# Optimization experiments

Measured on AMD Instinct MI355X. Metric: run time of the kernel, lower is better.

The kernel has to match this reference:

```python
import jax, jax.numpy as jnp
import numpy as np

BATCH, T, IN_DIM = 256, 1024, 96
N_UNITS, N_CLASSES = 256, 10
EPS, BETA, GAMMA = 0.01, 0.5, 0.0


def setup_inputs() -> dict:
    key = jax.random.key(0)
    k = jax.random.split(key, 7)
    # Xavier-ish scales for linear layers; unit gaussian for C, B (gaussian_init_ std=1)
    return {
        "x":   jax.random.normal(k[0], (BATCH, T, IN_DIM), dtype=jnp.float32),
        "E_w": jax.random.normal(k[1], (N_UNITS, IN_DIM), dtype=jnp.float32) * (2.0 / (IN_DIM + N_UNITS)) ** 0.5,
        "E_b": jnp.zeros((N_UNITS,), dtype=jnp.float32),
        "C":   jax.random.normal(k[2], (N_UNITS, N_UNITS), dtype=jnp.float32) / N_UNITS ** 0.5,
        "B":   jax.random.normal(k[3], (N_UNITS, N_UNITS), dtype=jnp.float32) / N_UNITS ** 0.5,
        "D_w": jax.random.normal(k[4], (N_CLASSES, N_UNITS), dtype=jnp.float32) * (2.0 / (N_UNITS + N_CLASSES)) ** 0.5,
        "D_b": jnp.zeros((N_CLASSES,), dtype=jnp.float32),
    }


def reference(x, E_w, E_b, C, B, D_w, D_b):
    # Invariant recurrence matrices (the torch code rebuilds these every step)
    I = jnp.eye(N_UNITS, dtype=x.dtype)
    A  = BETA * (C - C.T) + (1.0 - BETA) * (C + C.T) - GAMMA * I
    Dm = BETA * (B - B.T) + (1.0 - BETA) * (B + B.T) - GAMMA * I

    # Input projection for all timesteps at once: [B, T, N]
    z = jnp.einsum("btf,nf->btn", x, E_w) + E_b

    def step(h, z_t):  # h: [B, N], z_t: [B, N]
        h = h + EPS * (h @ Dm) + EPS * jnp.tanh(h @ A + z_t)
        return h, None

    h0 = jnp.zeros((x.shape[0], N_UNITS), dtype=x.dtype)
    h, _ = jax.lax.scan(step, h0, jnp.swapaxes(z, 0, 1))  # scan over T

    return h @ D_w.T + D_b  # [B, n_classes]
```

## Files before the change

### kernel.cpp

```cpp
#include <hip/hip_runtime.h>

#define BATCH 256
#define TT 1024
#define IN_DIM 96
#define NU 256
#define NC 10
#define EPS 0.01f
#define BETA 0.5f
#define GAMMA 0.0f

typedef _Float16 f16x8 __attribute__((ext_vector_type(8)));
typedef float f32x4 __attribute__((ext_vector_type(4)));

#define ZP_BYTES ((size_t)TT * BATCH * NU * 2)
#define WSW_OFF  ZP_BYTES
#define WSW_BYTES ((size_t)16384 * 16)
#define ESW_OFF  (WSW_OFF + WSW_BYTES)

__global__ void prep_w(const float* __restrict__ C, const float* __restrict__ B,
                       _Float16* __restrict__ Wsw) {
    int u = blockIdx.x * 256 + threadIdx.x;
    int l = u & 63;
    int i = (u >> 6) & 1;
    int c = (u >> 7) & 7;
    int mat = (u >> 10) & 1;
    int w = u >> 11;
    int n = w * 32 + i * 16 + (l & 15);
    int kb = c * 32 + (l >> 4) * 8;
    const float* M = mat ? C : B;
    float scale = mat ? 16.0f : EPS;
    f16x8 v;
#pragma unroll
    for (int j = 0; j < 8; j++) {
        int k = kb + j;
        float m1 = M[k * NU + n];
        float m2 = M[n * NU + k];
        float val = BETA * (m1 - m2) + (1.0f - BETA) * (m1 + m2)
                    - ((k == n) ? GAMMA : 0.0f);
        v[j] = (_Float16)(val * scale);
    }
    ((f16x8*)Wsw)[u] = v;
}

__global__ void prep_e(const float* __restrict__ Ew, _Float16* __restrict__ Esw) {
    int u = blockIdx.x * 256 + threadIdx.x;
    int l = u & 63;
    int i = (u >> 6) & 3;
    int wc = u >> 8;
    int c = wc % 3;
    int w = wc / 3;
    int n = w * 64 + i * 16 + (l & 15);
    int kb = c * 32 + (l >> 4) * 8;
    f16x8 v;
#pragma unroll
    for (int j = 0; j < 8; j++)
        v[j] = (_Float16)Ew[n * IN_DIM + kb + j];
    ((f16x8*)Esw)[u] = v;
}

__global__ __launch_bounds__(256) void zproj(const float* __restrict__ x,
                                             const float* __restrict__ Eb,
                                             const _Float16* __restrict__ Esw,
                                             _Float16* __restrict__ zp) {
    __shared__ __align__(16) _Float16 xh[64 * 104];
    __shared__ float eb[NU];
    int tid = threadIdx.x;
    int l = tid & 63, w = tid >> 6, m = l & 15, quad = l >> 4;
    size_t R0 = (size_t)blockIdx.x * 64;

    const float* xb = x + R0 * IN_DIM;
#pragma unroll
    for (int it = 0; it < 24; it++) {
        int idx = tid + it * 256;
        int r = idx / 96, k = idx - r * 96;
        xh[r * 104 + k] = (_Float16)xb[idx];
    }
    eb[tid] = Eb[tid];

    f16x8 ef[3][4];
    const f16x8* Ep = (const f16x8*)Esw;
#pragma unroll
    for (int c = 0; c < 3; c++)
#pragma unroll
        for (int i = 0; i < 4; i++)
            ef[c][i] = Ep[((w * 3 + c) * 4 + i) * 64 + l];
    __syncthreads();

    f32x4 zero4 = {0.f, 0.f, 0.f, 0.f};
    f32x4 acc[4][4];
#pragma unroll
    for (int mt = 0; mt < 4; mt++)
#pragma unroll
        for (int i = 0; i < 4; i++) acc[mt][i] = zero4;

#pragma unroll
    for (int mt = 0; mt < 4; mt++) {
#pragma unroll
        for (int c = 0; c < 3; c++) {
            f16x8 af = *(const f16x8*)&xh[(mt * 16 + m) * 104 + c * 32 + quad * 8];
#pragma unroll
            for (int i = 0; i < 4; i++)
                acc[mt][i] = __builtin_amdgcn_mfma_f32_16x16x32_f16(af, ef[c][i],
                                                                    acc[mt][i], 0, 0, 0);
        }
    }

#pragma unroll
    for (int mt = 0; mt < 4; mt++)
#pragma unroll
        for (int i = 0; i < 4; i++) {
            int col = w * 64 + i * 16 + m;
            float ebv = eb[col];
#pragma unroll
            for (int r = 0; r < 4; r++) {
                size_t gr = R0 + (size_t)(mt * 16 + quad * 4 + r);
                size_t b = gr >> 10, t = gr & 1023;
                zp[(t * BATCH + b) * NU + col] = (_Float16)(acc[mt][i][r] + ebv);
            }
        }
}


__device__ __forceinline__ void load_zchunk(_Float16 zb[2][8],
                                            const _Float16* __restrict__ zp,
                                            int tb, int zrow, int colb) {
#pragma unroll
    for (int s = 0; s < 2; s++) {
        int ts = tb + s; ts = (ts > TT - 1) ? TT - 1 : ts;
#pragma unroll
        for (int r = 0; r < 4; r++)
#pragma unroll
            for (int i = 0; i < 2; i++)
                zb[s][i * 4 + r] = zp[((size_t)ts * 256 + zrow + r) * 256 + colb + i * 16];
    }
}

__device__ __forceinline__ void step_fn(const _Float16* __restrict__ hb,
                                        _Float16* __restrict__ hn,
                                        const f16x8 wd[8][2], const f16x8 wa[8][2],
                                        float hm[8], const _Float16 zs[8],
                                        int m, int q, int w) {
    f32x4 faccD[2], faccA[2];
    f32x4 zero4 = {0.f, 0.f, 0.f, 0.f};
#pragma unroll
    for (int i = 0; i < 2; i++) {
        faccD[i] = zero4;
        f32x4 zi = {(float)zs[i * 4 + 0], (float)zs[i * 4 + 1],
                    (float)zs[i * 4 + 2], (float)zs[i * 4 + 3]};
        faccA[i] = zi;
    }

#pragma unroll
    for (int c = 0; c < 8; c++) {
        f16x8 af = *(const f16x8*)&hb[m * 264 + c * 32 + q * 8];
#pragma unroll
        for (int i = 0; i < 2; i++) {
            faccD[i] = __builtin_amdgcn_mfma_f32_16x16x32_f16(af, wd[c][i], faccD[i], 0, 0, 0);
            faccA[i] = __builtin_amdgcn_mfma_f32_16x16x32_f16(af, wa[c][i], faccA[i], 0, 0, 0);
        }
    }

#pragma unroll
    for (int i = 0; i < 2; i++) {
        int n = w * 32 + i * 16 + m;
#pragma unroll
        for (int r = 0; r < 4; r++) {
            int row = q * 4 + r;
            float xin = faccA[i][r];
            float e = __builtin_amdgcn_exp2f(xin * 2.8853900817779268f);
            float th = 1.0f - 2.0f * __builtin_amdgcn_rcpf(e + 1.0f);
            hm[i * 4 + r] += faccD[i][r] + (EPS * 0.0625f) * th;
            hn[row * 264 + n] = (_Float16)hm[i * 4 + r];
        }
    }
    __syncthreads();
}

__global__ __launch_bounds__(512, 2) void recur(const _Float16* __restrict__ Wsw,
                                                const _Float16* __restrict__ zp,
                                                const float* __restrict__ Dw,
                                                const float* __restrict__ Db,
                                                float* __restrict__ out) {
    __shared__ __align__(16) _Float16 hbuf0[16 * 264];
    __shared__ __align__(16) _Float16 hbuf1[16 * 264];
    __shared__ float Yep[16 * 257];
    int tid = threadIdx.x;
    int l = tid & 63, w = tid >> 6, m = l & 15, q = l >> 4;
    int wg = blockIdx.x;

    f16x8 wd[8][2], wa[8][2];
    const f16x8* Wp = (const f16x8*)Wsw;
#pragma unroll
    for (int c = 0; c < 8; c++)
#pragma unroll
        for (int i = 0; i < 2; i++) {
            wd[c][i] = Wp[(((w * 2 + 0) * 8 + c) * 2 + i) * 64 + l];
            wa[c][i] = Wp[(((w * 2 + 1) * 8 + c) * 2 + i) * 64 + l];
        }
#pragma unroll
    for (int c = 0; c < 8; c++)
#pragma unroll
        for (int i = 0; i < 2; i++)
            asm volatile("" : "+v"(wd[c][i]), "+v"(wa[c][i]));

    float hm[8];
#pragma unroll
    for (int e = 0; e < 8; e++) hm[e] = 0.0f;
    for (int idx = tid; idx < 16 * 264; idx += 512) hbuf0[idx] = (_Float16)0.0f;

    int zrow = wg * 16 + q * 4;
    int colb = w * 32 + m;
    _Float16 zA[2][8], zB[2][8];
    load_zchunk(zA, zp, 0, zrow, colb);
    load_zchunk(zB, zp, 2, zrow, colb);
    __syncthreads();

    for (int t = 0; t < TT; t += 4) {
        step_fn(hbuf0, hbuf1, wd, wa, hm, zA[0], m, q, w);
        step_fn(hbuf1, hbuf0, wd, wa, hm, zA[1], m, q, w);
        load_zchunk(zA, zp, t + 4, zrow, colb);
        step_fn(hbuf0, hbuf1, wd, wa, hm, zB[0], m, q, w);
        step_fn(hbuf1, hbuf0, wd, wa, hm, zB[1], m, q, w);
        load_zchunk(zB, zp, t + 6, zrow, colb);
    }

#pragma unroll
    for (int i = 0; i < 2; i++)
#pragma unroll
        for (int r = 0; r < 4; r++)
            Yep[(q * 4 + r) * 257 + w * 32 + i * 16 + m] = 16.0f * hm[i * 4 + r];
    __syncthreads();
    if (tid < 160) {
        int rr = tid / 10, c = tid - rr * 10;
        float s = Db[c];
        for (int k = 0; k < 256; k++) s += Yep[rr * 257 + k] * Dw[c * 256 + k];
        out[(wg * 16 + rr) * 10 + c] = s;
    }
}

extern "C" void kernel_launch(void* const* d_in, const int* in_sizes, int n_in,
                              void* d_out, int out_size, void* d_ws, size_t ws_size,
                              hipStream_t stream) {
    const float* x  = (const float*)d_in[0];
    const float* Ew = (const float*)d_in[1];
    const float* Eb = (const float*)d_in[2];
    const float* C  = (const float*)d_in[3];
    const float* B  = (const float*)d_in[4];
    const float* Dw = (const float*)d_in[5];
    const float* Db = (const float*)d_in[6];
    float* out = (float*)d_out;

    char* ws = (char*)d_ws;
    _Float16* zp  = (_Float16*)(ws);
    _Float16* Wsw = (_Float16*)(ws + WSW_OFF);
    _Float16* Esw = (_Float16*)(ws + ESW_OFF);

    hipLaunchKernelGGL(prep_w, dim3(64), dim3(256), 0, stream, C, B, Wsw);
    hipLaunchKernelGGL(prep_e, dim3(12), dim3(256), 0, stream, Ew, Esw);
    hipLaunchKernelGGL(zproj, dim3(4096), dim3(256), 0, stream, x, Eb, Esw, zp);
    hipLaunchKernelGGL(recur, dim3(16), dim3(512), 0, stream, Wsw, zp, Dw, Db, out);
}
```

Baseline: 1.083 ms.

## Store z projection in recurrence-native fragment layout for vectorized loads

The projection kernel now computes per (batch-tile, time-tile) blocks and writes z into a layout ordered by time, workgroup and column, with each MFMA fragment's four rows stored contiguously. The recurrence can then fetch z as two 8-byte vector loads instead of sixteen scattered 2-byte loads per step. The bias is folded into the accumulator init and the tanh update is algebraically rearranged to save an op. In exchange, zproj stages output through LDS and adds two barriers per timestep.

```diff
diff --git a/kernel.cpp b/kernel.cpp
--- a/kernel.cpp
+++ b/kernel.cpp
@@ -10,9 +10,10 @@
 #define GAMMA 0.0f
 
 typedef _Float16 f16x8 __attribute__((ext_vector_type(8)));
+typedef _Float16 f16x4 __attribute__((ext_vector_type(4)));
 typedef float f32x4 __attribute__((ext_vector_type(4)));
 
-#define ZP_BYTES ((size_t)TT * BATCH * NU * 2)
+#define ZP_BYTES ((size_t)TT * 16 * 256 * 16 * 2)
 #define WSW_OFF  ZP_BYTES
 #define WSW_BYTES ((size_t)16384 * 16)
 #define ESW_OFF  (WSW_OFF + WSW_BYTES)
@@ -62,20 +63,11 @@
                                              const float* __restrict__ Eb,
                                              const _Float16* __restrict__ Esw,
                                              _Float16* __restrict__ zp) {
-    __shared__ __align__(16) _Float16 xh[64 * 104];
-    __shared__ float eb[NU];
+    __shared__ __align__(16) _Float16 zt[2][256 * 24];
     int tid = threadIdx.x;
-    int l = tid & 63, w = tid >> 6, m = l & 15, quad = l >> 4;
-    size_t R0 = (size_t)blockIdx.x * 64;
-
-    const float* xb = x + R0 * IN_DIM;
-#pragma unroll
-    for (int it = 0; it < 24; it++) {
-        int idx = tid + it * 256;
-        int r = idx / 96, k = idx - r * 96;
-        xh[r * 104 + k] = (_Float16)xb[idx];
-    }
-    eb[tid] = Eb[tid];
+    int l = tid & 63, wz = tid >> 6, m = l & 15, q = l >> 4;
+    int bb = blockIdx.x & 15, tb = blockIdx.x >> 4;
+    int t0 = tb * 16, B0 = bb * 16;
 
     f16x8 ef[3][4];
     const f16x8* Ep = (const f16x8*)Esw;
@@ -83,70 +75,81 @@
     for (int c = 0; c < 3; c++)
 #pragma unroll
         for (int i = 0; i < 4; i++)
-            ef[c][i] = Ep[((w * 3 + c) * 4 + i) * 64 + l];
-    __syncthreads();
-
-    f32x4 zero4 = {0.f, 0.f, 0.f, 0.f};
-    f32x4 acc[4][4];
-#pragma unroll
-    for (int mt = 0; mt < 4; mt++)
-#pragma unroll
-        for (int i = 0; i < 4; i++) acc[mt][i] = zero4;
-
-#pragma unroll
-    for (int mt = 0; mt < 4; mt++) {
+            ef[c][i] = Ep[((wz * 3 + c) * 4 + i) * 64 + l];
+    float eb[4];
+#pragma unroll
+    for (int i = 0; i < 4; i++) eb[i] = Eb[wz * 64 + i * 16 + m];
+
+    const float* xbase = x + (size_t)(B0 + m) * TT * IN_DIM + q * 8;
+
+    for (int t = 0; t < 16; t++) {
+        f16x8 af[3];
 #pragma unroll
         for (int c = 0; c < 3; c++) {
-            f16x8 af = *(const f16x8*)&xh[(mt * 16 + m) * 104 + c * 32 + quad * 8];
+            const float* px = xbase + (size_t)(t0 + t) * IN_DIM + c * 32;
+            float4 v0 = *(const float4*)px;
+            float4 v1 = *(const float4*)(px + 4);
+            f16x8 a;
+            a[0] = (_Float16)v0.x; a[1] = (_Float16)v0.y;
+            a[2] = (_Float16)v0.z; a[3] = (_Float16)v0.w;
+            a[4] = (_Float16)v1.x; a[5] = (_Float16)v1.y;
+            a[6] = (_Float16)v1.z; a[7] = (_Float16)v1.w;
+            af[c] = a;
+        }
+        f32x4 acc[4];
+#pragma unroll
+        for (int i = 0; i < 4; i++) { f32x4 e4 = {eb[i], eb[i], eb[i], eb[i]}; acc[i] = e4; }
+#pragma unroll
+        for (int c = 0; c < 3; c++)
 #pragma unroll
             for (int i = 0; i < 4; i++)
-                acc[mt][i] = __builtin_amdgcn_mfma_f32_16x16x32_f16(af, ef[c][i],
-                                                                    acc[mt][i], 0, 0, 0);
-        }
-    }
-
-#pragma unroll
-    for (int mt = 0; mt < 4; mt++)
+                acc[i] = __builtin_amdgcn_mfma_f32_16x16x32_f16(af[c], ef[c][i], acc[i], 0, 0, 0);
+
+        _Float16* zb = zt[t & 1];
 #pragma unroll
         for (int i = 0; i < 4; i++) {
-            int col = w * 64 + i * 16 + m;
-            float ebv = eb[col];
-#pragma unroll
-            for (int r = 0; r < 4; r++) {
-                size_t gr = R0 + (size_t)(mt * 16 + quad * 4 + r);
-                size_t b = gr >> 10, t = gr & 1023;
-                zp[(t * BATCH + b) * NU + col] = (_Float16)(acc[mt][i][r] + ebv);
-            }
-        }
-}
-
-
-__device__ __forceinline__ void load_zchunk(_Float16 zb[2][8],
-                                            const _Float16* __restrict__ zp,
-                                            int tb, int zrow, int colb) {
+            f16x4 o = {(_Float16)acc[i][0], (_Float16)acc[i][1],
+                       (_Float16)acc[i][2], (_Float16)acc[i][3]};
+            *(f16x4*)&zb[(wz * 64 + i * 16 + m) * 24 + q * 4] = o;
+        }
+        __syncthreads();
+        {
+            _Float16* src = &zb[tid * 24];
+            f16x8 s0 = *(f16x8*)src;
+            f16x8 s1 = *(f16x8*)(src + 8);
+            _Float16* dst = zp + ((((size_t)(t0 + t) * 16) + bb) * 256 + tid) * 16;
+            *(f16x8*)dst = s0;
+            *(f16x8*)(dst + 8) = s1;
+        }
+        __syncthreads();
+    }
+}
+
+
+__device__ __forceinline__ void load_z2(f16x4 zc[2][2],
+                                        const _Float16* __restrict__ zp,
+                                        int tb, int wg, size_t voff0, size_t voff1) {
 #pragma unroll
     for (int s = 0; s < 2; s++) {
         int ts = tb + s; ts = (ts > TT - 1) ? TT - 1 : ts;
-#pragma unroll
-        for (int r = 0; r < 4; r++)
-#pragma unroll
-            for (int i = 0; i < 2; i++)
-                zb[s][i * 4 + r] = zp[((size_t)ts * 256 + zrow + r) * 256 + colb + i * 16];
+        const _Float16* pz = zp + ((size_t)ts * 16 + wg) * 4096;
+        zc[s][0] = *(const f16x4*)(pz + voff0);
+        zc[s][1] = *(const f16x4*)(pz + voff1);
     }
 }
 
 __device__ __forceinline__ void step_fn(const _Float16* __restrict__ hb,
                                         _Float16* __restrict__ hn,
                                         const f16x8 wd[8][2], const f16x8 wa[8][2],
-                                        float hm[8], const _Float16 zs[8],
+                                        float hm[8], const f16x4 zs[2],
                                         int m, int q, int w) {
     f32x4 faccD[2], faccA[2];
     f32x4 zero4 = {0.f, 0.f, 0.f, 0.f};
 #pragma unroll
     for (int i = 0; i < 2; i++) {
         faccD[i] = zero4;
-        f32x4 zi = {(float)zs[i * 4 + 0], (float)zs[i * 4 + 1],
-                    (float)zs[i * 4 + 2], (float)zs[i * 4 + 3]};
+        f32x4 zi = {(float)zs[i][0], (float)zs[i][1],
+                    (float)zs[i][2], (float)zs[i][3]};
         faccA[i] = zi;
     }
 
@@ -168,8 +171,9 @@
             int row = q * 4 + r;
             float xin = faccA[i][r];
             float e = __builtin_amdgcn_exp2f(xin * 2.8853900817779268f);
-            float th = 1.0f - 2.0f * __builtin_amdgcn_rcpf(e + 1.0f);
-            hm[i * 4 + r] += faccD[i][r] + (EPS * 0.0625f) * th;
+            float R = __builtin_amdgcn_rcpf(e + 1.0f);
+            float s = hm[i * 4 + r] + faccD[i][r];
+            hm[i * 4 + r] = s + (EPS * 0.0625f) - (2.0f * EPS * 0.0625f) * R;
             hn[row * 264 + n] = (_Float16)hm[i * 4 + r];
         }
     }
@@ -208,20 +212,20 @@
     for (int e = 0; e < 8; e++) hm[e] = 0.0f;
     for (int idx = tid; idx < 16 * 264; idx += 512) hbuf0[idx] = (_Float16)0.0f;
 
-    int zrow = wg * 16 + q * 4;
-    int colb = w * 32 + m;
-    _Float16 zA[2][8], zB[2][8];
-    load_zchunk(zA, zp, 0, zrow, colb);
-    load_zchunk(zB, zp, 2, zrow, colb);
+    size_t voff0 = (size_t)(w * 32 + m) * 16 + q * 4;
+    size_t voff1 = voff0 + 256;
+    f16x4 zA[2][2], zB[2][2];
+    load_z2(zA, zp, 0, wg, voff0, voff1);
+    load_z2(zB, zp, 2, wg, voff0, voff1);
     __syncthreads();
 
     for (int t = 0; t < TT; t += 4) {
         step_fn(hbuf0, hbuf1, wd, wa, hm, zA[0], m, q, w);
         step_fn(hbuf1, hbuf0, wd, wa, hm, zA[1], m, q, w);
-        load_zchunk(zA, zp, t + 4, zrow, colb);
+        load_z2(zA, zp, t + 4, wg, voff0, voff1);
         step_fn(hbuf0, hbuf1, wd, wa, hm, zB[0], m, q, w);
         step_fn(hbuf1, hbuf0, wd, wa, hm, zB[1], m, q, w);
-        load_zchunk(zB, zp, t + 6, zrow, colb);
+        load_z2(zB, zp, t + 6, wg, voff0, voff1);
     }
 
 #pragma unroll
@@ -257,6 +261,6 @@
 
     hipLaunchKernelGGL(prep_w, dim3(64), dim3(256), 0, stream, C, B, Wsw);
     hipLaunchKernelGGL(prep_e, dim3(12), dim3(256), 0, stream, Ew, Esw);
-    hipLaunchKernelGGL(zproj, dim3(4096), dim3(256), 0, stream, x, Eb, Esw, zp);
+    hipLaunchKernelGGL(zproj, dim3(1024), dim3(256), 0, stream, x, Eb, Esw, zp);
     hipLaunchKernelGGL(recur, dim3(16), dim3(512), 0, stream, Wsw, zp, Dw, Db, out);
 }
```

Result: no change. 1.079 ms (-0.4%).
